# Kernel optimization log

Hardware: AMD Instinct MI355X
Metric: run time of the kernel (lower is better)

Reference implementation:

```python
import jax, jax.numpy as jnp
import numpy as np

EPS = 1e-5  # torch default eps for both LayerNorm and BatchNorm
NH, KD, HD = 8, 16, 32  # num_heads, key_dim, head_dim for inc=256


def conv1x1(x, w, b=None):
    # w: [Cout, Cin]; x: [B, Cin, H, W]
    y = jnp.einsum('oc,bchw->bohw', w, x)
    return y if b is None else y + b[None, :, None, None]


def dwconv3x3(x, w, b=None):
    # depthwise 3x3, padding 1; w: [C, 1, 3, 3]
    C = x.shape[1]
    y = jax.lax.conv_general_dilated(x, w, (1, 1), ((1, 1), (1, 1)),
                                     dimension_numbers=('NCHW', 'OIHW', 'NCHW'),
                                     feature_group_count=C)
    return y if b is None else y + b[None, :, None, None]


def bn_eval(x, p):
    # p: [4, C] stacked (gamma, beta, running_mean, running_var); eval-mode BN
    g, b, m, v = p
    s = (g * jax.lax.rsqrt(v + EPS))[None, :, None, None]
    return (x - m[None, :, None, None]) * s + b[None, :, None, None]


def ln2d(x, g, b):
    # LayerNorm over channel dim (== permute->LN(C)->permute in torch)
    mu = x.mean(axis=1, keepdims=True)
    var = x.var(axis=1, keepdims=True)  # biased var, matches F.layer_norm
    return (x - mu) * jax.lax.rsqrt(var + EPS) * g[None, :, None, None] + b[None, :, None, None]


def setup_inputs() -> dict:
    key = jax.random.key(0)
    ks = jax.random.split(key, 20)
    B, C, H, W = 8, 256, 32, 32
    h_qkv = C + 2 * NH * KD  # 512
    hid = int(2 * C / 3)     # 170

    def bn_params(k, c):
        k1, k2, k3, k4 = jax.random.split(k, 4)
        g = 1.0 + 0.1 * jax.random.normal(k1, (c,), jnp.float32)
        b = 0.1 * jax.random.normal(k2, (c,), jnp.float32)
        m = 0.1 * jax.random.normal(k3, (c,), jnp.float32)
        v = jax.random.uniform(k4, (c,), jnp.float32, 0.5, 1.5)
        return jnp.stack([g, b, m, v])

    sc = lambda fan: 1.0 / np.sqrt(fan)
    return {
        'x': jax.random.normal(ks[0], (B, C, H, W), jnp.float32),
        'ln1_g': 1.0 + 0.1 * jax.random.normal(ks[1], (C,), jnp.float32),
        'ln1_b': 0.1 * jax.random.normal(ks[2], (C,), jnp.float32),
        'ln2_g': 1.0 + 0.1 * jax.random.normal(ks[3], (C,), jnp.float32),
        'ln2_b': 0.1 * jax.random.normal(ks[4], (C,), jnp.float32),
        'qkv_w': sc(C) * jax.random.normal(ks[5], (h_qkv, C), jnp.float32),
        'qkv_bn': bn_params(ks[6], h_qkv),
        'pe_w': sc(9) * jax.random.normal(ks[7], (C, 1, 3, 3), jnp.float32),
        'pe_bn': bn_params(ks[8], C),
        'proj_w': sc(C) * jax.random.normal(ks[9], (C, C), jnp.float32),
        'proj_bn': bn_params(ks[10], C),
        'fc1_w': sc(C) * jax.random.normal(ks[11], (2 * hid, C), jnp.float32),
        'fc1_b': 0.01 * jax.random.normal(ks[12], (2 * hid,), jnp.float32),
        'dw_w': sc(9) * jax.random.normal(ks[13], (hid, 1, 3, 3), jnp.float32),
        'dw_b': 0.01 * jax.random.normal(ks[14], (hid,), jnp.float32),
        'fc2_w': sc(hid) * jax.random.normal(ks[15], (C, hid), jnp.float32),
        'fc2_b': 0.01 * jax.random.normal(ks[16], (C,), jnp.float32),
    }


def reference(x, ln1_g, ln1_b, ln2_g, ln2_b, qkv_w, qkv_bn, pe_w, pe_bn,
              proj_w, proj_bn, fc1_w, fc1_b, dw_w, dw_b, fc2_w, fc2_b):
    B, C, H, W = x.shape
    N = H * W

    # --- PSA attention branch (eval mode: drop_path = identity) ---
    xn = ln2d(x, ln1_g, ln1_b)
    qkv = bn_eval(conv1x1(xn, qkv_w), qkv_bn)            # [B, 2*nh*kd + C, H, W]
    qkv = qkv.reshape(B, NH, 2 * KD + HD, N)
    q, k, v = qkv[:, :, :KD], qkv[:, :, KD:2 * KD], qkv[:, :, 2 * KD:]
    scale = KD ** -0.5
    attn = jax.nn.softmax(jnp.einsum('bhkn,bhkm->bhnm', q, k) * scale, axis=-1)
    o = jnp.einsum('bhdm,bhnm->bhdn', v, attn).reshape(B, C, H, W)
    o = o + bn_eval(dwconv3x3(v.reshape(B, C, H, W), pe_w), pe_bn)
    o = bn_eval(conv1x1(o, proj_w), proj_bn)
    x = x + o

    # --- Convolutional GLU branch (internal residual uses normed input) ---
    xn2 = ln2d(x, ln2_g, ln2_b)
    h = conv1x1(xn2, fc1_w, fc1_b)
    a, g = jnp.split(h, 2, axis=1)
    a = jax.nn.gelu(dwconv3x3(a, dw_w, dw_b), approximate=False) * g
    mlp_out = xn2 + conv1x1(a, fc2_w, fc2_b)
    return x + mlp_out
```

## Files before the change

kernel.cpp:

```cpp
#include <hip/hip_runtime.h>
#include <hip/hip_bf16.h>
#include <math.h>

#define EPSF 1e-5f

using short4v = __attribute__((ext_vector_type(4))) short;
using short8 = __attribute__((ext_vector_type(8))) short;
using f32x4 = __attribute__((ext_vector_type(4))) float;

__device__ inline short bfbits(float x) {
  __hip_bfloat16 h = __float2bfloat16(x);
  return __builtin_bit_cast(short, h);
}
__device__ inline float bf2f(short s) {
  unsigned u = ((unsigned)(unsigned short)s) << 16;
  return __builtin_bit_cast(float, u);
}

__global__ __launch_bounds__(256) void prep_kernel(
    const float* __restrict__ qkv_w, const float* __restrict__ qkv_bn,
    const float* __restrict__ proj_w, const float* __restrict__ proj_bn,
    const float* __restrict__ fc1_w, const float* __restrict__ fc2_w,
    const float* __restrict__ pe_w, const float* __restrict__ pe_bn,
    short* __restrict__ wq, float* __restrict__ bq, short* __restrict__ wpj,
    float* __restrict__ bpj, short* __restrict__ wf1, short* __restrict__ wf2,
    float* __restrict__ pw2, float* __restrict__ pb) {
  int id = blockIdx.x * 256 + threadIdx.x;
  if (id < 131072) {
    int o = id >> 8, k = id & 255;
    float g = qkv_bn[o], bb = qkv_bn[512 + o], m = qkv_bn[1024 + o],
          v = qkv_bn[1536 + o];
    float s = g * rsqrtf(v + EPSF);
    float s2 = ((o & 63) < 16) ? 0.25f : 1.0f;
    wq[id] = bfbits(qkv_w[id] * s * s2);
    if (k == 0) bq[o] = (bb - m * s) * s2;
  } else if (id < 196608) {
    int i = id - 131072;
    int o = i >> 8, k = i & 255;
    float g = proj_bn[o], bb = proj_bn[256 + o], m = proj_bn[512 + o],
          v = proj_bn[768 + o];
    float s = g * rsqrtf(v + EPSF);
    wpj[i] = bfbits(proj_w[i] * s);
    if (k == 0) bpj[o] = bb - m * s;
  } else if (id < 294912) {
    int i = id - 196608;
    int o = i >> 8, k = i & 255;
    wf1[i] = bfbits(o < 340 ? fc1_w[o * 256 + k] : 0.f);
  } else if (id < 344064) {
    int i = id - 294912;
    int o = i / 192, k = i - o * 192;
    wf2[i] = bfbits(k < 170 ? fc2_w[o * 170 + k] : 0.f);
  } else if (id < 346368) {
    int i = id - 344064;
    int c = i / 9;
    float g = pe_bn[c], bb = pe_bn[256 + c], m = pe_bn[512 + c],
          v = pe_bn[768 + c];
    float s = g * rsqrtf(v + EPSF);
    pw2[i] = pe_w[i] * s;
    if (i - c * 9 == 0) pb[c] = bb - m * s;
  }
}

__global__ __launch_bounds__(256) void ln1_kernel(
    const float* __restrict__ x, const float* __restrict__ gamma,
    const float* __restrict__ beta, short* __restrict__ xn) {
  __shared__ float s_sum[16][16];
  __shared__ float s_sq[16][16];
  int t = threadIdx.x;
  int nl = t & 15, cg = t >> 4;
  int p0 = blockIdx.x * 16;
  int b = p0 >> 10;
  int n = (p0 & 1023) + nl;
  const float* xp = x + ((size_t)b * 256 + cg * 16) * 1024 + n;
  float v[16];
  float sum = 0.f, sq = 0.f;
#pragma unroll
  for (int i = 0; i < 16; ++i) {
    float val = xp[(size_t)i * 1024];
    v[i] = val;
    sum += val;
    sq += val * val;
  }
  s_sum[cg][nl] = sum;
  s_sq[cg][nl] = sq;
  __syncthreads();
  float ts = 0.f, tq = 0.f;
#pragma unroll
  for (int g = 0; g < 16; ++g) {
    ts += s_sum[g][nl];
    tq += s_sq[g][nl];
  }
  float mu = ts * (1.f / 256.f);
  float var = tq * (1.f / 256.f) - mu * mu;
  float rs = rsqrtf(var + EPSF);
  short8 pk[2];
#pragma unroll
  for (int i = 0; i < 16; ++i) {
    int c = cg * 16 + i;
    pk[i >> 3][i & 7] = bfbits((v[i] - mu) * rs * gamma[c] + beta[c]);
  }
  short* op = xn + ((size_t)b * 1024 + n) * 256 + cg * 16;
  *reinterpret_cast<short8*>(op) = pk[0];
  *reinterpret_cast<short8*>(op + 8) = pk[1];
}

__global__ __launch_bounds__(256) void ln2_kernel(
    const float* __restrict__ x1, const float* __restrict__ gamma,
    const float* __restrict__ beta, short* __restrict__ xn2) {
  int t = threadIdx.x;
  int lane = t & 63, w = t >> 6;
  f32x4 gv = *reinterpret_cast<const f32x4*>(&gamma[lane * 4]);
  f32x4 bv = *reinterpret_cast<const f32x4*>(&beta[lane * 4]);
#pragma unroll
  for (int it = 0; it < 4; ++it) {
    size_t pos = blockIdx.x * 16 + w * 4 + it;
    f32x4 xv = *reinterpret_cast<const f32x4*>(&x1[pos * 256 + lane * 4]);
    float s = (xv[0] + xv[1]) + (xv[2] + xv[3]);
    float q = (xv[0] * xv[0] + xv[1] * xv[1]) + (xv[2] * xv[2] + xv[3] * xv[3]);
#pragma unroll
    for (int off = 1; off < 64; off <<= 1) {
      s += __shfl_xor(s, off);
      q += __shfl_xor(q, off);
    }
    float mu = s * (1.f / 256.f);
    float var = q * (1.f / 256.f) - mu * mu;
    float rs = rsqrtf(var + EPSF);
    short4v o;
#pragma unroll
    for (int e = 0; e < 4; ++e)
      o[e] = bfbits((xv[e] - mu) * rs * gv[e] + bv[e]);
    *reinterpret_cast<short4v*>(&xn2[pos * 256 + lane * 4]) = o;
  }
}

template <int MODE>
__global__ __launch_bounds__(256) void gemm2_kernel(
    const short* __restrict__ X, const short* __restrict__ W,
    const float* __restrict__ bias, const float* __restrict__ addCM,
    const float* __restrict__ add1CL, const short* __restrict__ add2CL,
    void* __restrict__ out, int OC, int K, int OT, int KS, int RS) {
  __shared__ short Wl[64][40];
  __shared__ short Xl[64][40];
  int bx = blockIdx.x;
  int ot = bx % OT;
  int ntb = bx / OT;
  int b = ntb >> 4;
  int n0 = (ntb & 15) * 64;
  int o0 = ot * 64;
  int t = threadIdx.x;
  int lane = t & 63, w = t >> 6;
  int wo = w >> 1, wn = w & 1;
  int g = lane >> 4, r = lane & 15;
  int srow = t >> 2, sk8 = (t & 3) * 8;
  size_t bN = (size_t)b * 1024;
  f32x4 acc[2][2] = {};
  int nsteps = K >> 5;
  for (int ks = 0; ks < nsteps; ++ks) {
    int k0 = ks << 5;
    __syncthreads();
    short8 wv = *reinterpret_cast<const short8*>(&W[(size_t)(o0 + srow) * K + k0 + sk8]);
    short8 xv = *reinterpret_cast<const short8*>(&X[(bN + n0 + srow) * KS + k0 + sk8]);
    *reinterpret_cast<short8*>(&Wl[srow][sk8]) = wv;
    *reinterpret_cast<short8*>(&Xl[srow][sk8]) = xv;
    __syncthreads();
    short8 a0 = *reinterpret_cast<const short8*>(&Wl[wo * 32 + r][g * 8]);
    short8 a1 = *reinterpret_cast<const short8*>(&Wl[wo * 32 + 16 + r][g * 8]);
    short8 b0 = *reinterpret_cast<const short8*>(&Xl[wn * 32 + r][g * 8]);
    short8 b1 = *reinterpret_cast<const short8*>(&Xl[wn * 32 + 16 + r][g * 8]);
    acc[0][0] = __builtin_amdgcn_mfma_f32_16x16x32_bf16(a0, b0, acc[0][0], 0, 0, 0);
    acc[0][1] = __builtin_amdgcn_mfma_f32_16x16x32_bf16(a0, b1, acc[0][1], 0, 0, 0);
    acc[1][0] = __builtin_amdgcn_mfma_f32_16x16x32_bf16(a1, b0, acc[1][0], 0, 0, 0);
    acc[1][1] = __builtin_amdgcn_mfma_f32_16x16x32_bf16(a1, b1, acc[1][1], 0, 0, 0);
  }
#pragma unroll
  for (int i = 0; i < 2; ++i) {
#pragma unroll
    for (int j = 0; j < 2; ++j) {
      int oq = o0 + wo * 32 + i * 16 + g * 4;
      if (oq >= OC) continue;
      int n = n0 + wn * 32 + j * 16 + r;
      f32x4 bv = *reinterpret_cast<const f32x4*>(&bias[oq]);
      f32x4 res;
#pragma unroll
      for (int rr = 0; rr < 4; ++rr) res[rr] = acc[i][j][rr] + bv[rr];
      if constexpr (MODE == 0) {
        short4v s;
#pragma unroll
        for (int rr = 0; rr < 4; ++rr) s[rr] = bfbits(res[rr]);
        *reinterpret_cast<short4v*>((short*)out + (bN + n) * RS + oq) = s;
      } else if constexpr (MODE == 1) {
#pragma unroll
        for (int rr = 0; rr < 4; ++rr)
          res[rr] += addCM[((size_t)b * 256 + oq + rr) * 1024 + n];
        *reinterpret_cast<f32x4*>((float*)out + (bN + n) * 256 + oq) = res;
      } else {
        f32x4 a1v = *reinterpret_cast<const f32x4*>(&add1CL[(bN + n) * 256 + oq]);
        short4v a2v = *reinterpret_cast<const short4v*>(&add2CL[(bN + n) * 256 + oq]);
#pragma unroll
        for (int rr = 0; rr < 4; ++rr) {
          float v = res[rr] + a1v[rr] + bf2f(a2v[rr]);
          ((float*)out)[((size_t)b * 256 + oq + rr) * 1024 + n] = v;
        }
      }
    }
  }
}

__global__ __launch_bounds__(256) void attn2_kernel(
    const short* __restrict__ qkv, float* __restrict__ ob) {
  __shared__ short Ql[64][40];
  __shared__ short Kl[64][40];
  __shared__ short Vl[32][72];
  int blk = blockIdx.x;
  int qt = blk & 15, h = (blk >> 4) & 7, b = blk >> 7;
  const short* base = qkv + (size_t)b * 1024 * 512 + h * 64;
  int t = threadIdx.x;
  int lane = t & 63, w = t >> 6;
  int g = lane >> 4, r = lane & 15;
  int q0 = qt * 64;
  for (int i = t; i < 64 * 16; i += 256) {
    int row = i >> 4, col = 16 + (i & 15);
    Ql[row][col] = 0;
    Kl[row][col] = 0;
  }
  {
    int qr = t >> 2, kd4 = (t & 3) * 4;
    short4v qv = *reinterpret_cast<const short4v*>(&base[(size_t)(q0 + qr) * 512 + kd4]);
    *reinterpret_cast<short4v*>(&Ql[qr][kd4]) = qv;
  }
  __syncthreads();
  short8 qf = *reinterpret_cast<const short8*>(&Ql[w * 16 + r][g * 8]);
  float M = -3e38f, l = 0.f;
  f32x4 O0 = {}, O1 = {};
  int mr4 = t >> 2, kd4 = (t & 3) * 4;
  int mrv = t & 63, dg = t >> 6;
  for (int ch = 0; ch < 16; ++ch) {
    int m0 = ch * 64;
    {
      short4v kv = *reinterpret_cast<const short4v*>(
          &base[(size_t)(m0 + mr4) * 512 + 16 + kd4]);
      *reinterpret_cast<short4v*>(&Kl[mr4][kd4]) = kv;
    }
    {
      short8 vv = *reinterpret_cast<const short8*>(
          &base[(size_t)(m0 + mrv) * 512 + 32 + dg * 8]);
#pragma unroll
      for (int e = 0; e < 8; ++e) Vl[dg * 8 + e][mrv] = vv[e];
    }
    __syncthreads();
    f32x4 s[4];
#pragma unroll
    for (int mt = 0; mt < 4; ++mt) {
      short8 af = *reinterpret_cast<const short8*>(&Kl[mt * 16 + r][g * 8]);
      f32x4 z = {};
      s[mt] = __builtin_amdgcn_mfma_f32_16x16x32_bf16(af, qf, z, 0, 0, 0);
    }
    float mx = -3e38f;
#pragma unroll
    for (int mt = 0; mt < 4; ++mt)
      mx = fmaxf(mx, fmaxf(fmaxf(s[mt][0], s[mt][1]), fmaxf(s[mt][2], s[mt][3])));
    mx = fmaxf(mx, __shfl_xor(mx, 16));
    mx = fmaxf(mx, __shfl_xor(mx, 32));
    float Mn = fmaxf(M, mx);
    float f = __expf(M - Mn);
    M = Mn;
    float sc = 0.f;
    short8 pa[4];
#pragma unroll
    for (int mt = 0; mt < 4; ++mt) {
      float p0 = __expf(s[mt][0] - Mn);
      float p1 = __expf(s[mt][1] - Mn);
      float p2 = __expf(s[mt][2] - Mn);
      float p3 = __expf(s[mt][3] - Mn);
      sc += (p0 + p1) + (p2 + p3);
      pa[mt] = (short8){bfbits(p0), bfbits(p1), bfbits(p2), bfbits(p3),
                        0, 0, 0, 0};
    }
    sc += __shfl_xor(sc, 16);
    sc += __shfl_xor(sc, 32);
    l = l * f + sc;
#pragma unroll
    for (int rr = 0; rr < 4; ++rr) {
      float fr = __shfl(f, g * 4 + rr);
      O0[rr] *= fr;
      O1[rr] *= fr;
    }
#pragma unroll
    for (int mt = 0; mt < 4; ++mt) {
      short4v v0 = *reinterpret_cast<const short4v*>(&Vl[r][mt * 16 + g * 4]);
      short4v v1 = *reinterpret_cast<const short4v*>(&Vl[16 + r][mt * 16 + g * 4]);
      short8 b0 = {v0[0], v0[1], v0[2], v0[3], 0, 0, 0, 0};
      short8 b1 = {v1[0], v1[1], v1[2], v1[3], 0, 0, 0, 0};
      O0 = __builtin_amdgcn_mfma_f32_16x16x32_bf16(pa[mt], b0, O0, 0, 0, 0);
      O1 = __builtin_amdgcn_mfma_f32_16x16x32_bf16(pa[mt], b1, O1, 0, 0, 0);
    }
    __syncthreads();
  }
  float* obp = ob + ((size_t)b * 1024 + q0 + w * 16) * 256 + h * 32;
#pragma unroll
  for (int rr = 0; rr < 4; ++rr) {
    float lr = __shfl(l, g * 4 + rr);
    float inv = 1.f / lr;
    size_t qoff = (size_t)(g * 4 + rr) * 256;
    obp[qoff + r] = O0[rr] * inv;
    obp[qoff + 16 + r] = O1[rr] * inv;
  }
}

__global__ __launch_bounds__(256) void pe2_kernel(
    const short* __restrict__ qkv, const float* __restrict__ pw2,
    const float* __restrict__ pb, const float* __restrict__ ob,
    short* __restrict__ obf) {
  int idx = blockIdx.x * 256 + threadIdx.x;
  int c = idx & 255;
  int n = (idx >> 8) & 1023;
  int b = idx >> 18;
  int y = n >> 5, xx = n & 31;
  int head = c >> 5, d = c & 31;
  const short* v = qkv + (size_t)b * 1024 * 512 + head * 64 + 32 + d;
  const float* wp = pw2 + c * 9;
  float s = pb[c];
#pragma unroll
  for (int dy = -1; dy <= 1; ++dy) {
    int yy = y + dy;
    if (yy < 0 || yy > 31) continue;
#pragma unroll
    for (int dx = -1; dx <= 1; ++dx) {
      int xw = xx + dx;
      if (xw < 0 || xw > 31) continue;
      s += wp[(dy + 1) * 3 + (dx + 1)] * bf2f(v[(size_t)(yy * 32 + xw) * 512]);
    }
  }
  obf[idx] = bfbits(ob[idx] + s);
}

__global__ __launch_bounds__(192) void glu2_kernel(
    const short* __restrict__ h, const float* __restrict__ dw_w,
    const float* __restrict__ dw_b, short* __restrict__ act) {
  int n = blockIdx.x & 1023;
  int b = blockIdx.x >> 10;
  int t = threadIdx.x;
  short* arow = act + ((size_t)b * 1024 + n) * 192;
  if (t >= 170) {
    arow[t] = 0;
    return;
  }
  int y = n >> 5, xx = n & 31;
  const short* hb = h + (size_t)b * 1024 * 352;
  const float* wp = dw_w + t * 9;
  float s = dw_b[t];
#pragma unroll
  for (int dy = -1; dy <= 1; ++dy) {
    int yy = y + dy;
    if (yy < 0 || yy > 31) continue;
#pragma unroll
    for (int dx = -1; dx <= 1; ++dx) {
      int xw = xx + dx;
      if (xw < 0 || xw > 31) continue;
      s += wp[(dy + 1) * 3 + (dx + 1)] * bf2f(hb[(size_t)(yy * 32 + xw) * 352 + t]);
    }
  }
  float ge = 0.5f * s * (1.f + erff(s * 0.70710678118654752f));
  float gv = bf2f(hb[(size_t)n * 352 + 170 + t]);
  arow[t] = bfbits(ge * gv);
}

extern "C" void kernel_launch(void* const* d_in, const int* in_sizes, int n_in,
                              void* d_out, int out_size, void* d_ws,
                              size_t ws_size, hipStream_t stream) {
  const float* x      = (const float*)d_in[0];
  const float* ln1_g  = (const float*)d_in[1];
  const float* ln1_b  = (const float*)d_in[2];
  const float* ln2_g  = (const float*)d_in[3];
  const float* ln2_b  = (const float*)d_in[4];
  const float* qkv_w  = (const float*)d_in[5];
  const float* qkv_bn = (const float*)d_in[6];
  const float* pe_w   = (const float*)d_in[7];
  const float* pe_bn  = (const float*)d_in[8];
  const float* proj_w = (const float*)d_in[9];
  const float* proj_bn= (const float*)d_in[10];
  const float* fc1_w  = (const float*)d_in[11];
  const float* fc1_b  = (const float*)d_in[12];
  const float* dw_w   = (const float*)d_in[13];
  const float* dw_b   = (const float*)d_in[14];
  const float* fc2_w  = (const float*)d_in[15];
  const float* fc2_b  = (const float*)d_in[16];

  char* base = (char*)d_ws;
  short* xn   = (short*)(base + 0);
  short* qkv  = (short*)(base + 4194304);
  float* ob   = (float*)(base + 12582912);
  short* obf  = (short*)(base + 20971520);
  float* x1   = (float*)(base + 25165824);
  short* xn2  = (short*)(base + 33554432);
  short* hbuf = (short*)(base + 37748736);
  short* act  = (short*)(base + 43515904);
  short* wq   = (short*)(base + 46661632);
  short* wpj  = (short*)(base + 46923776);
  short* wf1  = (short*)(base + 47054848);
  short* wf2  = (short*)(base + 47251456);
  float* pw2  = (float*)(base + 47349760);
  float* pb   = (float*)(base + 47358976);
  float* bq   = (float*)(base + 47360000);
  float* bpj  = (float*)(base + 47362048);
  float* outp = (float*)d_out;

  hipLaunchKernelGGL(prep_kernel, dim3(1353), dim3(256), 0, stream, qkv_w,
                     qkv_bn, proj_w, proj_bn, fc1_w, fc2_w, pe_w, pe_bn, wq,
                     bq, wpj, bpj, wf1, wf2, pw2, pb);
  hipLaunchKernelGGL(ln1_kernel, dim3(512), dim3(256), 0, stream, x, ln1_g,
                     ln1_b, xn);
  hipLaunchKernelGGL((gemm2_kernel<0>), dim3(1024), dim3(256), 0, stream, xn,
                     wq, bq, nullptr, nullptr, nullptr, qkv, 512, 256, 8, 256,
                     512);
  hipLaunchKernelGGL(attn2_kernel, dim3(1024), dim3(256), 0, stream, qkv, ob);
  hipLaunchKernelGGL(pe2_kernel, dim3(8192), dim3(256), 0, stream, qkv, pw2,
                     pb, ob, obf);
  hipLaunchKernelGGL((gemm2_kernel<1>), dim3(512), dim3(256), 0, stream, obf,
                     wpj, bpj, x, nullptr, nullptr, x1, 256, 256, 4, 256, 256);
  hipLaunchKernelGGL(ln2_kernel, dim3(512), dim3(256), 0, stream, x1, ln2_g,
                     ln2_b, xn2);
  hipLaunchKernelGGL((gemm2_kernel<0>), dim3(768), dim3(256), 0, stream, xn2,
                     wf1, fc1_b, nullptr, nullptr, nullptr, hbuf, 340, 256, 6,
                     256, 352);
  hipLaunchKernelGGL(glu2_kernel, dim3(8192), dim3(192), 0, stream, hbuf,
                     dw_w, dw_b, act);
  hipLaunchKernelGGL((gemm2_kernel<2>), dim3(512), dim3(256), 0, stream, act,
                     wf2, fc2_b, nullptr, x1, xn2, outp, 256, 192, 4, 192,
                     256);
}
```

Before: 205.9 us.

## Fuse positional dwconv into attention, widen GEMM tiles with register prefetch, vectorize GLU

```diff
diff --git a/kernel.cpp b/kernel.cpp
--- a/kernel.cpp
+++ b/kernel.cpp
@@ -4,6 +4,7 @@
 
 #define EPSF 1e-5f
 
+using short2v = __attribute__((ext_vector_type(2))) short;
 using short4v = __attribute__((ext_vector_type(4))) short;
 using short8 = __attribute__((ext_vector_type(8))) short;
 using f32x4 = __attribute__((ext_vector_type(4))) float;
@@ -22,9 +23,11 @@
     const float* __restrict__ proj_w, const float* __restrict__ proj_bn,
     const float* __restrict__ fc1_w, const float* __restrict__ fc2_w,
     const float* __restrict__ pe_w, const float* __restrict__ pe_bn,
+    const float* __restrict__ dw_w, const float* __restrict__ dw_b,
     short* __restrict__ wq, float* __restrict__ bq, short* __restrict__ wpj,
     float* __restrict__ bpj, short* __restrict__ wf1, short* __restrict__ wf2,
-    float* __restrict__ pw2, float* __restrict__ pb) {
+    float* __restrict__ pwT, float* __restrict__ pbv, float* __restrict__ wdT,
+    float* __restrict__ dbv) {
   int id = blockIdx.x * 256 + threadIdx.x;
   if (id < 131072) {
     int o = id >> 8, k = id & 255;
@@ -52,12 +55,17 @@
     wf2[i] = bfbits(k < 170 ? fc2_w[o * 170 + k] : 0.f);
   } else if (id < 346368) {
     int i = id - 344064;
-    int c = i / 9;
+    int c = i & 255, tap = i >> 8;
     float g = pe_bn[c], bb = pe_bn[256 + c], m = pe_bn[512 + c],
           v = pe_bn[768 + c];
     float s = g * rsqrtf(v + EPSF);
-    pw2[i] = pe_w[i] * s;
-    if (i - c * 9 == 0) pb[c] = bb - m * s;
+    pwT[tap * 256 + c] = pe_w[c * 9 + tap] * s;
+    if (tap == 0) pbv[c] = bb - m * s;
+  } else if (id < 348096) {
+    int i = id - 346368;
+    int c = i % 192, tap = i / 192;
+    wdT[tap * 192 + c] = (c < 170) ? dw_w[c * 9 + tap] : 0.f;
+    if (tap == 0) dbv[c] = (c < 170) ? dw_b[c] : 0.f;
   }
 }
 
@@ -134,49 +142,64 @@
 }
 
 template <int MODE>
-__global__ __launch_bounds__(256) void gemm2_kernel(
+__global__ __launch_bounds__(256) void gemm3_kernel(
     const short* __restrict__ X, const short* __restrict__ W,
     const float* __restrict__ bias, const float* __restrict__ addCM,
     const float* __restrict__ add1CL, const short* __restrict__ add2CL,
     void* __restrict__ out, int OC, int K, int OT, int KS, int RS) {
-  __shared__ short Wl[64][40];
+  __shared__ short Wl[128][40];
   __shared__ short Xl[64][40];
   int bx = blockIdx.x;
   int ot = bx % OT;
   int ntb = bx / OT;
   int b = ntb >> 4;
   int n0 = (ntb & 15) * 64;
-  int o0 = ot * 64;
+  int o0 = ot * 128;
   int t = threadIdx.x;
   int lane = t & 63, w = t >> 6;
   int wo = w >> 1, wn = w & 1;
   int g = lane >> 4, r = lane & 15;
   int srow = t >> 2, sk8 = (t & 3) * 8;
   size_t bN = (size_t)b * 1024;
-  f32x4 acc[2][2] = {};
+  const short* Wp0 = W + (size_t)(o0 + srow) * K + sk8;
+  const short* Wp1 = W + (size_t)(o0 + 64 + srow) * K + sk8;
+  const short* Xp = X + (bN + n0 + srow) * KS + sk8;
+  f32x4 acc[4][2] = {};
   int nsteps = K >> 5;
+  short8 w0 = *reinterpret_cast<const short8*>(Wp0);
+  short8 w1 = *reinterpret_cast<const short8*>(Wp1);
+  short8 x0 = *reinterpret_cast<const short8*>(Xp);
   for (int ks = 0; ks < nsteps; ++ks) {
-    int k0 = ks << 5;
+    *reinterpret_cast<short8*>(&Wl[srow][sk8]) = w0;
+    *reinterpret_cast<short8*>(&Wl[64 + srow][sk8]) = w1;
+    *reinterpret_cast<short8*>(&Xl[srow][sk8]) = x0;
     __syncthreads();
-    short8 wv = *reinterpret_cast<const short8*>(&W[(size_t)(o0 + srow) * K + k0 + sk8]);
-    short8 xv = *reinterpret_cast<const short8*>(&X[(bN + n0 + srow) * KS + k0 + sk8]);
-    *reinterpret_cast<short8*>(&Wl[srow][sk8]) = wv;
-    *reinterpret_cast<short8*>(&Xl[srow][sk8]) = xv;
+    if (ks + 1 < nsteps) {
+      int ko = (ks + 1) << 5;
+      w0 = *reinterpret_cast<const short8*>(Wp0 + ko);
+      w1 = *reinterpret_cast<const short8*>(Wp1 + ko);
+      x0 = *reinterpret_cast<const short8*>(Xp + ko);
+    }
+    short8 a[4], bb[2];
+#pragma unroll
+    for (int i = 0; i < 4; ++i)
+      a[i] = *reinterpret_cast<const short8*>(&Wl[wo * 64 + i * 16 + r][g * 8]);
+#pragma unroll
+    for (int j = 0; j < 2; ++j)
+      bb[j] = *reinterpret_cast<const short8*>(&Xl[wn * 32 + j * 16 + r][g * 8]);
+#pragma unroll
+    for (int i = 0; i < 4; ++i)
+#pragma unroll
+      for (int j = 0; j < 2; ++j)
+        acc[i][j] = __builtin_amdgcn_mfma_f32_16x16x32_bf16(a[i], bb[j],
+                                                            acc[i][j], 0, 0, 0);
     __syncthreads();
-    short8 a0 = *reinterpret_cast<const short8*>(&Wl[wo * 32 + r][g * 8]);
-    short8 a1 = *reinterpret_cast<const short8*>(&Wl[wo * 32 + 16 + r][g * 8]);
-    short8 b0 = *reinterpret_cast<const short8*>(&Xl[wn * 32 + r][g * 8]);
-    short8 b1 = *reinterpret_cast<const short8*>(&Xl[wn * 32 + 16 + r][g * 8]);
-    acc[0][0] = __builtin_amdgcn_mfma_f32_16x16x32_bf16(a0, b0, acc[0][0], 0, 0, 0);
-    acc[0][1] = __builtin_amdgcn_mfma_f32_16x16x32_bf16(a0, b1, acc[0][1], 0, 0, 0);
-    acc[1][0] = __builtin_amdgcn_mfma_f32_16x16x32_bf16(a1, b0, acc[1][0], 0, 0, 0);
-    acc[1][1] = __builtin_amdgcn_mfma_f32_16x16x32_bf16(a1, b1, acc[1][1], 0, 0, 0);
-  }
-#pragma unroll
-  for (int i = 0; i < 2; ++i) {
+  }
+#pragma unroll
+  for (int i = 0; i < 4; ++i) {
 #pragma unroll
     for (int j = 0; j < 2; ++j) {
-      int oq = o0 + wo * 32 + i * 16 + g * 4;
+      int oq = o0 + wo * 64 + i * 16 + g * 4;
       if (oq >= OC) continue;
       int n = n0 + wn * 32 + j * 16 + r;
       f32x4 bv = *reinterpret_cast<const f32x4*>(&bias[oq]);
@@ -206,14 +229,17 @@
   }
 }
 
-__global__ __launch_bounds__(256) void attn2_kernel(
-    const short* __restrict__ qkv, float* __restrict__ ob) {
+__global__ __launch_bounds__(256) void attn3_kernel(
+    const short* __restrict__ qkv, const float* __restrict__ pwT,
+    const float* __restrict__ pbv, short* __restrict__ obf) {
   __shared__ short Ql[64][40];
   __shared__ short Kl[64][40];
   __shared__ short Vl[32][72];
+  __shared__ short Ol[64][36];
   int blk = blockIdx.x;
   int qt = blk & 15, h = (blk >> 4) & 7, b = blk >> 7;
-  const short* base = qkv + (size_t)b * 1024 * 512 + h * 64;
+  size_t bN = (size_t)b * 1024;
+  const short* base = qkv + bN * 512 + h * 64;
   int t = threadIdx.x;
   int lane = t & 63, w = t >> 6;
   int g = lane >> 4, r = lane & 15;
@@ -225,7 +251,8 @@
   }
   {
     int qr = t >> 2, kd4 = (t & 3) * 4;
-    short4v qv = *reinterpret_cast<const short4v*>(&base[(size_t)(q0 + qr) * 512 + kd4]);
+    short4v qv =
+        *reinterpret_cast<const short4v*>(&base[(size_t)(q0 + qr) * 512 + kd4]);
     *reinterpret_cast<short4v*>(&Ql[qr][kd4]) = qv;
   }
   __syncthreads();
@@ -233,32 +260,42 @@
   float M = -3e38f, l = 0.f;
   f32x4 O0 = {}, O1 = {};
   int mr4 = t >> 2, kd4 = (t & 3) * 4;
-  int mrv = t & 63, dg = t >> 6;
+  int mp = t & 31, dq8 = t >> 5;
+  short4v kreg =
+      *reinterpret_cast<const short4v*>(&base[(size_t)mr4 * 512 + 16 + kd4]);
+  short4v vA = *reinterpret_cast<const short4v*>(
+      &base[(size_t)(2 * mp) * 512 + 32 + dq8 * 4]);
+  short4v vB = *reinterpret_cast<const short4v*>(
+      &base[(size_t)(2 * mp + 1) * 512 + 32 + dq8 * 4]);
   for (int ch = 0; ch < 16; ++ch) {
-    int m0 = ch * 64;
-    {
-      short4v kv = *reinterpret_cast<const short4v*>(
+    *reinterpret_cast<short4v*>(&Kl[mr4][kd4]) = kreg;
+#pragma unroll
+    for (int e = 0; e < 4; ++e) {
+      short2v p = {vA[e], vB[e]};
+      *reinterpret_cast<short2v*>(&Vl[dq8 * 4 + e][2 * mp]) = p;
+    }
+    __syncthreads();
+    if (ch + 1 < 16) {
+      int m0 = (ch + 1) * 64;
+      kreg = *reinterpret_cast<const short4v*>(
           &base[(size_t)(m0 + mr4) * 512 + 16 + kd4]);
-      *reinterpret_cast<short4v*>(&Kl[mr4][kd4]) = kv;
-    }
-    {
-      short8 vv = *reinterpret_cast<const short8*>(
-          &base[(size_t)(m0 + mrv) * 512 + 32 + dg * 8]);
-#pragma unroll
-      for (int e = 0; e < 8; ++e) Vl[dg * 8 + e][mrv] = vv[e];
-    }
-    __syncthreads();
-    f32x4 s[4];
+      vA = *reinterpret_cast<const short4v*>(
+          &base[(size_t)(m0 + 2 * mp) * 512 + 32 + dq8 * 4]);
+      vB = *reinterpret_cast<const short4v*>(
+          &base[(size_t)(m0 + 2 * mp + 1) * 512 + 32 + dq8 * 4]);
+    }
+    f32x4 s4[4];
 #pragma unroll
     for (int mt = 0; mt < 4; ++mt) {
       short8 af = *reinterpret_cast<const short8*>(&Kl[mt * 16 + r][g * 8]);
       f32x4 z = {};
-      s[mt] = __builtin_amdgcn_mfma_f32_16x16x32_bf16(af, qf, z, 0, 0, 0);
+      s4[mt] = __builtin_amdgcn_mfma_f32_16x16x32_bf16(af, qf, z, 0, 0, 0);
     }
     float mx = -3e38f;
 #pragma unroll
     for (int mt = 0; mt < 4; ++mt)
-      mx = fmaxf(mx, fmaxf(fmaxf(s[mt][0], s[mt][1]), fmaxf(s[mt][2], s[mt][3])));
+      mx = fmaxf(mx,
+                 fmaxf(fmaxf(s4[mt][0], s4[mt][1]), fmaxf(s4[mt][2], s4[mt][3])));
     mx = fmaxf(mx, __shfl_xor(mx, 16));
     mx = fmaxf(mx, __shfl_xor(mx, 32));
     float Mn = fmaxf(M, mx);
@@ -268,10 +305,10 @@
     short8 pa[4];
 #pragma unroll
     for (int mt = 0; mt < 4; ++mt) {
-      float p0 = __expf(s[mt][0] - Mn);
-      float p1 = __expf(s[mt][1] - Mn);
-      float p2 = __expf(s[mt][2] - Mn);
-      float p3 = __expf(s[mt][3] - Mn);
+      float p0 = __expf(s4[mt][0] - Mn);
+      float p1 = __expf(s4[mt][1] - Mn);
+      float p2 = __expf(s4[mt][2] - Mn);
+      float p3 = __expf(s4[mt][3] - Mn);
       sc += (p0 + p1) + (p2 + p3);
       pa[mt] = (short8){bfbits(p0), bfbits(p1), bfbits(p2), bfbits(p3),
                         0, 0, 0, 0};
@@ -288,7 +325,8 @@
 #pragma unroll
     for (int mt = 0; mt < 4; ++mt) {
       short4v v0 = *reinterpret_cast<const short4v*>(&Vl[r][mt * 16 + g * 4]);
-      short4v v1 = *reinterpret_cast<const short4v*>(&Vl[16 + r][mt * 16 + g * 4]);
+      short4v v1 =
+          *reinterpret_cast<const short4v*>(&Vl[16 + r][mt * 16 + g * 4]);
       short8 b0 = {v0[0], v0[1], v0[2], v0[3], 0, 0, 0, 0};
       short8 b1 = {v1[0], v1[1], v1[2], v1[3], 0, 0, 0, 0};
       O0 = __builtin_amdgcn_mfma_f32_16x16x32_bf16(pa[mt], b0, O0, 0, 0, 0);
@@ -296,30 +334,60 @@
     }
     __syncthreads();
   }
-  float* obp = ob + ((size_t)b * 1024 + q0 + w * 16) * 256 + h * 32;
 #pragma unroll
   for (int rr = 0; rr < 4; ++rr) {
     float lr = __shfl(l, g * 4 + rr);
     float inv = 1.f / lr;
-    size_t qoff = (size_t)(g * 4 + rr) * 256;
-    obp[qoff + r] = O0[rr] * inv;
-    obp[qoff + 16 + r] = O1[rr] * inv;
-  }
-}
-
-__global__ __launch_bounds__(256) void pe2_kernel(
-    const short* __restrict__ qkv, const float* __restrict__ pw2,
-    const float* __restrict__ pb, const float* __restrict__ ob,
-    short* __restrict__ obf) {
-  int idx = blockIdx.x * 256 + threadIdx.x;
-  int c = idx & 255;
-  int n = (idx >> 8) & 1023;
-  int b = idx >> 18;
+    int q = w * 16 + g * 4 + rr;
+    Ol[q][r] = bfbits(O0[rr] * inv);
+    Ol[q][16 + r] = bfbits(O1[rr] * inv);
+  }
+  __syncthreads();
+#pragma unroll
+  for (int it = 0; it < 2; ++it) {
+    int item = t + it * 256;
+    int q = item & 63, dq = item >> 6;
+    int n = q0 + q;
+    int y = n >> 5, xx = n & 31;
+    int cq = h * 32 + dq * 4;
+    f32x4 s = *reinterpret_cast<const f32x4*>(&pbv[cq]);
+#pragma unroll
+    for (int dy = -1; dy <= 1; ++dy) {
+      int yy = y + dy;
+      if (yy < 0 || yy > 31) continue;
+#pragma unroll
+      for (int dx = -1; dx <= 1; ++dx) {
+        int xw = xx + dx;
+        if (xw < 0 || xw > 31) continue;
+        int tap = (dy + 1) * 3 + (dx + 1);
+        f32x4 wv = *reinterpret_cast<const f32x4*>(&pwT[tap * 256 + cq]);
+        short4v vv = *reinterpret_cast<const short4v*>(
+            &base[(size_t)(yy * 32 + xw) * 512 + 32 + dq * 4]);
+#pragma unroll
+        for (int e = 0; e < 4; ++e) s[e] += wv[e] * bf2f(vv[e]);
+      }
+    }
+    short4v ov = *reinterpret_cast<const short4v*>(&Ol[q][dq * 4]);
+    short4v res;
+#pragma unroll
+    for (int e = 0; e < 4; ++e) res[e] = bfbits(bf2f(ov[e]) + s[e]);
+    *reinterpret_cast<short4v*>(&obf[(bN + n) * 256 + cq]) = res;
+  }
+}
+
+__global__ __launch_bounds__(256) void glu3_kernel(
+    const short* __restrict__ h, const float* __restrict__ wdT,
+    const float* __restrict__ dbv, short* __restrict__ act) {
+  int t = threadIdx.x;
+  int pos = blockIdx.x * 16 + (t >> 4);
+  int c0 = (t & 15) * 12;
+  int n = pos & 1023;
+  int b = pos >> 10;
   int y = n >> 5, xx = n & 31;
-  int head = c >> 5, d = c & 31;
-  const short* v = qkv + (size_t)b * 1024 * 512 + head * 64 + 32 + d;
-  const float* wp = pw2 + c * 9;
-  float s = pb[c];
+  const short* hb = h + (size_t)b * 1024 * 352;
+  float s[12];
+#pragma unroll
+  for (int e = 0; e < 12; ++e) s[e] = dbv[c0 + e];
 #pragma unroll
   for (int dy = -1; dy <= 1; ++dy) {
     int yy = y + dy;
@@ -328,41 +396,31 @@
     for (int dx = -1; dx <= 1; ++dx) {
       int xw = xx + dx;
       if (xw < 0 || xw > 31) continue;
-      s += wp[(dy + 1) * 3 + (dx + 1)] * bf2f(v[(size_t)(yy * 32 + xw) * 512]);
-    }
-  }
-  obf[idx] = bfbits(ob[idx] + s);
-}
-
-__global__ __launch_bounds__(192) void glu2_kernel(
-    const short* __restrict__ h, const float* __restrict__ dw_w,
-    const float* __restrict__ dw_b, short* __restrict__ act) {
-  int n = blockIdx.x & 1023;
-  int b = blockIdx.x >> 10;
-  int t = threadIdx.x;
-  short* arow = act + ((size_t)b * 1024 + n) * 192;
-  if (t >= 170) {
-    arow[t] = 0;
-    return;
-  }
-  int y = n >> 5, xx = n & 31;
-  const short* hb = h + (size_t)b * 1024 * 352;
-  const float* wp = dw_w + t * 9;
-  float s = dw_b[t];
-#pragma unroll
-  for (int dy = -1; dy <= 1; ++dy) {
-    int yy = y + dy;
-    if (yy < 0 || yy > 31) continue;
-#pragma unroll
-    for (int dx = -1; dx <= 1; ++dx) {
-      int xw = xx + dx;
-      if (xw < 0 || xw > 31) continue;
-      s += wp[(dy + 1) * 3 + (dx + 1)] * bf2f(hb[(size_t)(yy * 32 + xw) * 352 + t]);
-    }
-  }
-  float ge = 0.5f * s * (1.f + erff(s * 0.70710678118654752f));
-  float gv = bf2f(hb[(size_t)n * 352 + 170 + t]);
-  arow[t] = bfbits(ge * gv);
+      int tap = (dy + 1) * 3 + (dx + 1);
+      const float* wp = wdT + tap * 192 + c0;
+      const short* ap = hb + (size_t)(yy * 32 + xw) * 352 + c0;
+#pragma unroll
+      for (int v4 = 0; v4 < 3; ++v4) {
+        short4v av = *reinterpret_cast<const short4v*>(ap + v4 * 4);
+        f32x4 wv = *reinterpret_cast<const f32x4*>(wp + v4 * 4);
+#pragma unroll
+        for (int e = 0; e < 4; ++e) s[v4 * 4 + e] += wv[e] * bf2f(av[e]);
+      }
+    }
+  }
+  const short* gp = hb + (size_t)n * 352 + 170 + c0;
+  short* arow = act + ((size_t)b * 1024 + n) * 192 + c0;
+#pragma unroll
+  for (int v4 = 0; v4 < 3; ++v4) {
+    short4v res;
+#pragma unroll
+    for (int e = 0; e < 4; ++e) {
+      float sv = s[v4 * 4 + e];
+      float ge = 0.5f * sv * (1.f + erff(sv * 0.70710678118654752f));
+      res[e] = bfbits(ge * bf2f(gp[v4 * 4 + e]));
+    }
+    *reinterpret_cast<short4v*>(arow + v4 * 4) = res;
+  }
 }
 
 extern "C" void kernel_launch(void* const* d_in, const int* in_sizes, int n_in,
@@ -389,43 +447,43 @@
   char* base = (char*)d_ws;
   short* xn   = (short*)(base + 0);
   short* qkv  = (short*)(base + 4194304);
-  float* ob   = (float*)(base + 12582912);
-  short* obf  = (short*)(base + 20971520);
-  float* x1   = (float*)(base + 25165824);
-  short* xn2  = (short*)(base + 33554432);
-  short* hbuf = (short*)(base + 37748736);
-  short* act  = (short*)(base + 43515904);
-  short* wq   = (short*)(base + 46661632);
-  short* wpj  = (short*)(base + 46923776);
-  short* wf1  = (short*)(base + 47054848);
-  short* wf2  = (short*)(base + 47251456);
-  float* pw2  = (float*)(base + 47349760);
-  float* pb   = (float*)(base + 47358976);
-  float* bq   = (float*)(base + 47360000);
-  float* bpj  = (float*)(base + 47362048);
+  short* obf  = (short*)(base + 12582912);
+  float* x1   = (float*)(base + 16777216);
+  short* xn2  = (short*)(base + 25165824);
+  short* hbuf = (short*)(base + 29360128);
+  short* act  = (short*)(base + 35131392);
+  short* wq   = (short*)(base + 38277120);
+  short* wpj  = (short*)(base + 38539264);
+  short* wf1  = (short*)(base + 38670336);
+  short* wf2  = (short*)(base + 38866944);
+  float* pwT  = (float*)(base + 38965248);
+  float* pbv  = (float*)(base + 38974464);
+  float* wdT  = (float*)(base + 38975488);
+  float* dbv  = (float*)(base + 38982400);
+  float* bq   = (float*)(base + 38983168);
+  float* bpj  = (float*)(base + 38985216);
   float* outp = (float*)d_out;
 
-  hipLaunchKernelGGL(prep_kernel, dim3(1353), dim3(256), 0, stream, qkv_w,
-                     qkv_bn, proj_w, proj_bn, fc1_w, fc2_w, pe_w, pe_bn, wq,
-                     bq, wpj, bpj, wf1, wf2, pw2, pb);
+  hipLaunchKernelGGL(prep_kernel, dim3(1360), dim3(256), 0, stream, qkv_w,
+                     qkv_bn, proj_w, proj_bn, fc1_w, fc2_w, pe_w, pe_bn, dw_w,
+                     dw_b, wq, bq, wpj, bpj, wf1, wf2, pwT, pbv, wdT, dbv);
   hipLaunchKernelGGL(ln1_kernel, dim3(512), dim3(256), 0, stream, x, ln1_g,
                      ln1_b, xn);
-  hipLaunchKernelGGL((gemm2_kernel<0>), dim3(1024), dim3(256), 0, stream, xn,
-                     wq, bq, nullptr, nullptr, nullptr, qkv, 512, 256, 8, 256,
+  hipLaunchKernelGGL((gemm3_kernel<0>), dim3(512), dim3(256), 0, stream, xn,
+                     wq, bq, nullptr, nullptr, nullptr, qkv, 512, 256, 4, 256,
                      512);
-  hipLaunchKernelGGL(attn2_kernel, dim3(1024), dim3(256), 0, stream, qkv, ob);
-  hipLaunchKernelGGL(pe2_kernel, dim3(8192), dim3(256), 0, stream, qkv, pw2,
-                     pb, ob, obf);
-  hipLaunchKernelGGL((gemm2_kernel<1>), dim3(512), dim3(256), 0, stream, obf,
-                     wpj, bpj, x, nullptr, nullptr, x1, 256, 256, 4, 256, 256);
+  hipLaunchKernelGGL(attn3_kernel, dim3(1024), dim3(256), 0, stream, qkv, pwT,
+                     pbv, obf);
+  hipLaunchKernelGGL((gemm3_kernel<1>), dim3(256), dim3(256), 0, stream, obf,
+                     wpj, bpj, x, nullptr, nullptr, x1, 256, 256, 2, 256, 256);
   hipLaunchKernelGGL(ln2_kernel, dim3(512), dim3(256), 0, stream, x1, ln2_g,
                      ln2_b, xn2);
-  hipLaunchKernelGGL((gemm2_kernel<0>), dim3(768), dim3(256), 0, stream, xn2,
-                     wf1, fc1_b, nullptr, nullptr, nullptr, hbuf, 340, 256, 6,
+  hipLaunchKernelGGL((gemm3_kernel<0>), dim3(384), dim3(256), 0, stream, xn2,
+                     wf1, fc1_b, nullptr, nullptr, nullptr, hbuf, 340, 256, 3,
                      256, 352);
-  hipLaunchKernelGGL(glu2_kernel, dim3(8192), dim3(192), 0, stream, hbuf,
-                     dw_w, dw_b, act);
-  hipLaunchKernelGGL((gemm2_kernel<2>), dim3(512), dim3(256), 0, stream, act,
-                     wf2, fc2_b, nullptr, x1, xn2, outp, 256, 192, 4, 192,
+  hipLaunchKernelGGL(glu3_kernel, dim3(512), dim3(256), 0, stream, hbuf, wdT,
+                     dbv, act);
+  hipLaunchKernelGGL((gemm3_kernel<2>), dim3(256), dim3(256), 0, stream, act,
+                     wf2, fc2_b, nullptr, x1, xn2, outp, 256, 192, 2, 192,
                      256);
 }
```

New measurement: 182.6 us. 1.13x faster.
